# Kernel optimization log

Measured on AMD Instinct MI355X. Metric: run time of the kernel, lower is better.

Reference implementation:

```python
import jax, jax.numpy as jnp
import numpy as np

HEADS = 8  # head_dim = 512 // 8 = 64


def setup_inputs() -> dict:
    key = jax.random.key(0)
    ks = jax.random.split(key, 6)
    B, S, D = 1, 4096, 512
    s = 0.02
    return {
        "hidden_states": jax.random.normal(ks[0], (B, S, D), dtype=jnp.float32),
        "Wq": jax.random.normal(ks[1], (D, D), dtype=jnp.float32) * s,
        "Wk": jax.random.normal(ks[2], (D, D), dtype=jnp.float32) * s,
        "Wv": jax.random.normal(ks[3], (D, D), dtype=jnp.float32) * s,
        "Wo": jax.random.normal(ks[4], (D, D), dtype=jnp.float32) * s,
        "b_out": jnp.zeros((D,), dtype=jnp.float32),
    }


def reference(hidden_states, Wq, Wk, Wv, Wo, b_out):
    B, S, D = hidden_states.shape
    H = HEADS
    hd = D // H
    scale = 1.0 / jnp.sqrt(jnp.asarray(hd, hidden_states.dtype))

    # unfused QKV projections (self-attention, no mask)
    q = hidden_states @ Wq  # [B,S,D]
    k = hidden_states @ Wk
    v = hidden_states @ Wv

    # head_to_batch_dim: [B,S,D] -> [B,H,S,hd]
    def split_heads(t):
        return t.reshape(B, S, H, hd).transpose(0, 2, 1, 3)

    q, k, v = split_heads(q), split_heads(k), split_heads(v)

    # explicit score matrix + softmax (faithful to torch.bmm path)
    scores = jnp.einsum("bhqd,bhkd->bhqk", q, k) * scale  # [B,H,S,S]
    probs = jax.nn.softmax(scores, axis=-1)
    out = jnp.einsum("bhqk,bhkd->bhqd", probs, v)  # [B,H,S,hd]

    # batch_to_head_dim: [B,H,S,hd] -> [B,S,D]
    out = out.transpose(0, 2, 1, 3).reshape(B, S, D)
    # to_out[0] Linear + to_out[1] Dropout (identity at eval)
    return out @ Wo + b_out
```

## Files before the change

kernel.cpp:

```cpp
#include <hip/hip_runtime.h>
#include <hip/hip_bf16.h>

#define S_LEN 4096
#define DMODEL 512
#define NHEADS 8
#define HDIM 64

typedef __hip_bfloat16 bf16;
typedef __attribute__((ext_vector_type(8))) short bf16x8;
typedef __attribute__((ext_vector_type(4))) float f32x4;
typedef __attribute__((ext_vector_type(4))) _Float16 f16x4;
typedef __attribute__((ext_vector_type(8))) _Float16 f16x8;

__device__ __forceinline__ f32x4 mfma16x16x32(bf16x8 a, bf16x8 b, f32x4 c) {
    return __builtin_amdgcn_mfma_f32_16x16x32_bf16(a, b, c, 0, 0, 0);
}
__device__ __forceinline__ f32x4 mfma16x16x16h(f16x4 a, f16x4 b, f32x4 c) {
    return __builtin_amdgcn_mfma_f32_16x16x16f16(a, b, c, 0, 0, 0);
}
__device__ __forceinline__ void gload_lds16(const void* g, void* l) {
    __builtin_amdgcn_global_load_lds(
        (const __attribute__((address_space(1))) unsigned int*)g,
        (__attribute__((address_space(3))) unsigned int*)l, 16, 0, 0);
}

__global__ __launch_bounds__(256) void prep(
    const float* __restrict__ X,
    const float* __restrict__ Wq, const float* __restrict__ Wk,
    const float* __restrict__ Wv, const float* __restrict__ Wo,
    bf16* __restrict__ Xb, bf16* __restrict__ Wt)
{
    __shared__ bf16 tile[32][33];
    const int b = blockIdx.x;
    if (b < 1024) {
        int i = (b * 256 + threadIdx.x) * 8;
        float4 a = *(const float4*)(X + i);
        float4 c = *(const float4*)(X + i + 4);
        bf16 tmp[8];
        tmp[0] = __float2bfloat16(a.x); tmp[1] = __float2bfloat16(a.y);
        tmp[2] = __float2bfloat16(a.z); tmp[3] = __float2bfloat16(a.w);
        tmp[4] = __float2bfloat16(c.x); tmp[5] = __float2bfloat16(c.y);
        tmp[6] = __float2bfloat16(c.z); tmp[7] = __float2bfloat16(c.w);
        *(bf16x8*)(Xb + i) = *(bf16x8*)tmp;
    } else {
        const int bb = b - 1024;
        const int z = bb >> 8;
        const int bx = bb & 15, by = (bb >> 4) & 15;
        const float* src = (z == 0) ? Wq : (z == 1) ? Wk : (z == 2) ? Wv : Wo;
        bf16* dst = Wt + (size_t)z * DMODEL * DMODEL;
        const int tx = threadIdx.x & 31, ty = threadIdx.x >> 5;
        const int x = bx * 32 + tx;
        const int y0 = by * 32;
        #pragma unroll
        for (int i = ty; i < 32; i += 8)
            tile[i][tx] = __float2bfloat16(src[(size_t)(y0 + i) * DMODEL + x]);
        __syncthreads();
        const int xo = y0 + tx;
        #pragma unroll
        for (int i = ty; i < 32; i += 8)
            dst[(size_t)(bx * 32 + i) * DMODEL + xo] = tile[tx][i];
    }
}

__global__ __launch_bounds__(256) void gemm_qkv(
    const bf16* __restrict__ A, const bf16* __restrict__ Bt,
    bf16* __restrict__ Qm, bf16* __restrict__ Km, _Float16* __restrict__ Vt)
{
    __shared__ __align__(16) bf16 As[128 * 64];
    __shared__ __align__(16) bf16 Bs[128 * 64];
    const int m0 = blockIdx.x * 128, n0 = blockIdx.y * 128;
    const int t = threadIdx.x, lane = t & 63, w = t >> 6;
    const int lr = lane & 15, lq = lane >> 4;
    const int wr = w >> 1, wc = w & 1;

    f32x4 acc[4][4];
    #pragma unroll
    for (int i = 0; i < 4; ++i)
        #pragma unroll
        for (int j = 0; j < 4; ++j) acc[i][j] = f32x4{0, 0, 0, 0};

    const int srow = w * 32 + (lane >> 3);
    const int scol = (lane & 7) * 8;
    const bf16* Ab = A + (size_t)(m0 + srow) * DMODEL + scol;
    const bf16* Bb = Bt + (size_t)(n0 + srow) * DMODEL + scol;

    for (int k0 = 0; k0 < DMODEL; k0 += 64) {
        __syncthreads();
        #pragma unroll
        for (int i = 0; i < 4; ++i) {
            gload_lds16(Ab + (size_t)(i * 8) * DMODEL + k0, &As[(w * 32 + i * 8) * 64]);
            gload_lds16(Bb + (size_t)(i * 8) * DMODEL + k0, &Bs[(w * 32 + i * 8) * 64]);
        }
        __syncthreads();
        #pragma unroll
        for (int kc = 0; kc < 2; ++kc) {
            bf16x8 af[4], bfr[4];
            #pragma unroll
            for (int fq = 0; fq < 4; ++fq)
                af[fq] = *(const bf16x8*)&As[(wr * 64 + fq * 16 + lr) * 64 + kc * 32 + lq * 8];
            #pragma unroll
            for (int fr = 0; fr < 4; ++fr)
                bfr[fr] = *(const bf16x8*)&Bs[(wc * 64 + fr * 16 + lr) * 64 + kc * 32 + lq * 8];
            #pragma unroll
            for (int fq = 0; fq < 4; ++fq)
                #pragma unroll
                for (int fr = 0; fr < 4; ++fr)
                    acc[fq][fr] = mfma16x16x32(af[fq], bfr[fr], acc[fq][fr]);
        }
    }

    const int which = n0 >> 9;
    const int nloc = n0 & 511;
    const int row0 = m0 + wr * 64 + lq * 4;
    const int col0 = nloc + wc * 64 + lr;
    if (which == 0) {
        #pragma unroll
        for (int fq = 0; fq < 4; ++fq)
            #pragma unroll
            for (int fr = 0; fr < 4; ++fr)
                #pragma unroll
                for (int r = 0; r < 4; ++r)
                    Qm[(size_t)(row0 + fq * 16 + r) * DMODEL + col0 + fr * 16] =
                        __float2bfloat16(acc[fq][fr][r] * 0.18033688f);
    } else if (which == 1) {
        #pragma unroll
        for (int fq = 0; fq < 4; ++fq)
            #pragma unroll
            for (int fr = 0; fr < 4; ++fr)
                #pragma unroll
                for (int r = 0; r < 4; ++r)
                    Km[(size_t)(row0 + fq * 16 + r) * DMODEL + col0 + fr * 16] =
                        __float2bfloat16(acc[fq][fr][r]);
    } else {
        #pragma unroll
        for (int fq = 0; fq < 4; ++fq)
            #pragma unroll
            for (int fr = 0; fr < 4; ++fr) {
                _Float16 tmp[4];
                #pragma unroll
                for (int r = 0; r < 4; ++r) tmp[r] = (_Float16)acc[fq][fr][r];
                *(f16x4*)(Vt + (size_t)(col0 + fr * 16) * S_LEN + row0 + fq * 16) =
                    *(f16x4*)tmp;
            }
    }
}

__global__ __launch_bounds__(256) void gemm_out(
    const bf16* __restrict__ A, const bf16* __restrict__ Bt,
    float* __restrict__ Out, const float* __restrict__ bias)
{
    __shared__ __align__(16) bf16 As[128 * 64];
    __shared__ __align__(16) bf16 Bs[128 * 64];
    const int m0 = blockIdx.x * 128, n0 = blockIdx.y * 128;
    const int t = threadIdx.x, lane = t & 63, w = t >> 6;
    const int lr = lane & 15, lq = lane >> 4;
    const int wr = w >> 1, wc = w & 1;

    f32x4 acc[4][4];
    #pragma unroll
    for (int i = 0; i < 4; ++i)
        #pragma unroll
        for (int j = 0; j < 4; ++j) acc[i][j] = f32x4{0, 0, 0, 0};

    const int srow = w * 32 + (lane >> 3);
    const int scol = (lane & 7) * 8;
    const bf16* Ab = A + (size_t)(m0 + srow) * DMODEL + scol;
    const bf16* Bb = Bt + (size_t)(n0 + srow) * DMODEL + scol;

    for (int k0 = 0; k0 < DMODEL; k0 += 64) {
        __syncthreads();
        #pragma unroll
        for (int i = 0; i < 4; ++i) {
            gload_lds16(Ab + (size_t)(i * 8) * DMODEL + k0, &As[(w * 32 + i * 8) * 64]);
            gload_lds16(Bb + (size_t)(i * 8) * DMODEL + k0, &Bs[(w * 32 + i * 8) * 64]);
        }
        __syncthreads();
        #pragma unroll
        for (int kc = 0; kc < 2; ++kc) {
            bf16x8 af[4], bfr[4];
            #pragma unroll
            for (int fq = 0; fq < 4; ++fq)
                af[fq] = *(const bf16x8*)&As[(wr * 64 + fq * 16 + lr) * 64 + kc * 32 + lq * 8];
            #pragma unroll
            for (int fr = 0; fr < 4; ++fr)
                bfr[fr] = *(const bf16x8*)&Bs[(wc * 64 + fr * 16 + lr) * 64 + kc * 32 + lq * 8];
            #pragma unroll
            for (int fq = 0; fq < 4; ++fq)
                #pragma unroll
                for (int fr = 0; fr < 4; ++fr)
                    acc[fq][fr] = mfma16x16x32(af[fq], bfr[fr], acc[fq][fr]);
        }
    }

    const int row0 = m0 + wr * 64 + lq * 4;
    const int col0 = n0 + wc * 64 + lr;
    #pragma unroll
    for (int fq = 0; fq < 4; ++fq)
        #pragma unroll
        for (int fr = 0; fr < 4; ++fr)
            #pragma unroll
            for (int r = 0; r < 4; ++r)
                Out[(size_t)(row0 + fq * 16 + r) * DMODEL + col0 + fr * 16] =
                    acc[fq][fr][r] + bias[col0 + fr * 16];
}

__global__ __launch_bounds__(256, 2) void attn_kernel(
    const bf16* __restrict__ Q, const bf16* __restrict__ Kmat,
    const _Float16* __restrict__ Vt, bf16* __restrict__ Oout)
{
    __shared__ __align__(16) char smem[65536];

    const int h = blockIdx.x, qb = blockIdx.y;
    const int t = threadIdx.x, lane = t & 63, w = t >> 6;
    const int lr = lane & 15, lq = lane >> 4;
    const int q0 = qb * 64;

    char* myK = smem + w * 16384;
    char* myV = myK + 8192;

    const int sr = lane >> 3;
    const int scc = (lane & 7) ^ sr;
    const bf16*     gK = Kmat + (size_t)sr * DMODEL + h * HDIM + scc * 8;
    const _Float16* gV = Vt + (size_t)(h * HDIM + sr) * S_LEN + scc * 8;

    bf16x8 qf[4][2];
    #pragma unroll
    for (int qt = 0; qt < 4; ++qt) {
        const bf16* qp = Q + (size_t)(q0 + qt * 16 + lr) * DMODEL + h * HDIM + lq * 8;
        qf[qt][0] = *(const bf16x8*)qp;
        qf[qt][1] = *(const bf16x8*)(qp + 32);
    }

    f32x4 oacc[4][4];
    #pragma unroll
    for (int i = 0; i < 4; ++i)
        #pragma unroll
        for (int j = 0; j < 4; ++j) oacc[i][j] = f32x4{0, 0, 0, 0};
    float lsum[4] = {0, 0, 0, 0};

    #pragma unroll
    for (int i = 0; i < 8; ++i) {
        gload_lds16(gK + (size_t)(w * 64 + i * 8) * DMODEL, myK + i * 1024);
        gload_lds16(gV + (size_t)(i * 8) * S_LEN + w * 64, myV + i * 1024);
    }

    const int swz = (lr & 7) << 4;

    for (int kt = w; kt < S_LEN / 64; kt += 4) {
        asm volatile("s_waitcnt vmcnt(0)" ::: "memory");

        bf16x8 kf[4][2];
        #pragma unroll
        for (int mt = 0; mt < 4; ++mt) {
            const char* kr = myK + (mt * 16 + lr) * 128;
            kf[mt][0] = *(const bf16x8*)(kr + ((lq * 16) ^ swz));
            kf[mt][1] = *(const bf16x8*)(kr + ((64 + lq * 16) ^ swz));
        }
        f16x4 vf[4][4];
        #pragma unroll
        for (int ht = 0; ht < 4; ++ht) {
            const char* vr = myV + (ht * 16 + lr) * 128;
            #pragma unroll
            for (int mt = 0; mt < 4; ++mt)
                vf[mt][ht] = *(const f16x4*)(vr + ((mt * 32 + lq * 8) ^ swz));
        }
        asm volatile("s_waitcnt lgkmcnt(0)" ::: "memory");
        __builtin_amdgcn_sched_barrier(0);

        const int ktn = kt + 4;
        if (ktn < S_LEN / 64) {
            #pragma unroll
            for (int i = 0; i < 8; ++i) {
                gload_lds16(gK + (size_t)(ktn * 64 + i * 8) * DMODEL, myK + i * 1024);
                gload_lds16(gV + (size_t)(i * 8) * S_LEN + ktn * 64, myV + i * 1024);
            }
        }

        __builtin_amdgcn_s_setprio(1);
        f16x4 pf[4][4];
        #pragma unroll
        for (int qt = 0; qt < 4; ++qt) {
            f32x4 st[4];
            #pragma unroll
            for (int mt = 0; mt < 4; ++mt) {
                f32x4 z = {0, 0, 0, 0};
                z = mfma16x16x32(kf[mt][0], qf[qt][0], z);
                z = mfma16x16x32(kf[mt][1], qf[qt][1], z);
                st[mt] = z;
            }
            #pragma unroll
            for (int mt = 0; mt < 4; ++mt)
                #pragma unroll
                for (int r = 0; r < 4; ++r) {
                    float p = __builtin_amdgcn_exp2f(st[mt][r]);
                    lsum[qt] += p;
                    pf[qt][mt][r] = (_Float16)p;
                }
        }
        #pragma unroll
        for (int qt = 0; qt < 4; ++qt)
            #pragma unroll
            for (int ht = 0; ht < 4; ++ht)
                #pragma unroll
                for (int mt = 0; mt < 4; ++mt)
                    oacc[qt][ht] = mfma16x16x16h(pf[qt][mt], vf[mt][ht], oacc[qt][ht]);
        __builtin_amdgcn_s_setprio(0);
    }

    __syncthreads();
    float (*obuf)[3][4][64][4] = (float(*)[3][4][64][4])smem;
    float (*lbuf)[4][16]       = (float(*)[4][16])(smem + 49152);

    #pragma unroll
    for (int qt = 0; qt < 4; ++qt) {
        if (qt != w) {
            int j = qt - (qt > w ? 1 : 0);
            #pragma unroll
            for (int ht = 0; ht < 4; ++ht)
                *(f32x4*)&obuf[w][j][ht][lane][0] = oacc[qt][ht];
        }
    }
    #pragma unroll
    for (int qt = 0; qt < 4; ++qt) {
        float s = lsum[qt];
        s += __shfl_xor(s, 16);
        s += __shfl_xor(s, 32);
        if (lq == 0) lbuf[w][qt][lr] = s;
    }
    __syncthreads();

    f32x4 osum[4];
    #pragma unroll
    for (int qt = 0; qt < 4; ++qt)
        if (qt == w) {
            #pragma unroll
            for (int ht = 0; ht < 4; ++ht) osum[ht] = oacc[qt][ht];
        }
    #pragma unroll
    for (int w2 = 0; w2 < 4; ++w2) {
        if (w2 == w) continue;
        int j = w - (w > w2 ? 1 : 0);
        #pragma unroll
        for (int ht = 0; ht < 4; ++ht)
            osum[ht] += *(const f32x4*)&obuf[w2][j][ht][lane][0];
    }
    float linv[4];
    #pragma unroll
    for (int r = 0; r < 4; ++r) {
        int rr = lq * 4 + r;
        linv[r] = 1.0f / (lbuf[0][w][rr] + lbuf[1][w][rr] + lbuf[2][w][rr] + lbuf[3][w][rr]);
    }
    #pragma unroll
    for (int r = 0; r < 4; ++r) {
        int row = q0 + w * 16 + lq * 4 + r;
        #pragma unroll
        for (int ht = 0; ht < 4; ++ht)
            Oout[(size_t)row * DMODEL + h * HDIM + ht * 16 + lr] =
                __float2bfloat16(osum[ht][r] * linv[r]);
    }
}

extern "C" void kernel_launch(void* const* d_in, const int* in_sizes, int n_in,
                              void* d_out, int out_size, void* d_ws, size_t ws_size,
                              hipStream_t stream) {
    const float* X  = (const float*)d_in[0];
    const float* Wq = (const float*)d_in[1];
    const float* Wk = (const float*)d_in[2];
    const float* Wv = (const float*)d_in[3];
    const float* Wo = (const float*)d_in[4];
    const float* bo = (const float*)d_in[5];
    float* out = (float*)d_out;

    char* ws = (char*)d_ws;
    bf16* Wt = (bf16*)ws;
    bf16* Xb = (bf16*)(ws + (size_t)4 * DMODEL * DMODEL * 2);
    bf16* Qm = Xb + (size_t)S_LEN * DMODEL;
    bf16* Km = Qm + (size_t)S_LEN * DMODEL;
    _Float16* Vt = (_Float16*)(Km + (size_t)S_LEN * DMODEL);
    bf16* AO = (bf16*)(Vt + (size_t)S_LEN * DMODEL);

    bf16* Wot = Wt + (size_t)3 * DMODEL * DMODEL;

    prep<<<2048, 256, 0, stream>>>(X, Wq, Wk, Wv, Wo, Xb, Wt);

    gemm_qkv<<<dim3(S_LEN / 128, 3 * DMODEL / 128), 256, 0, stream>>>(
        Xb, Wt, Qm, Km, Vt);

    attn_kernel<<<dim3(NHEADS, S_LEN / 64), 256, 0, stream>>>(Qm, Km, Vt, AO);

    gemm_out<<<dim3(S_LEN / 128, DMODEL / 128), 256, 0, stream>>>(AO, Wot, out, bo);
}
```

Measured before the change: 139.5 us.

## Shrink GEMM tiles with double buffering, MFMA row sums, vectorized V loads

Both projection GEMMs move from 128x128 to 64x64 tiles with a double-buffered LDS prefetch pipeline, giving more blocks to fill the many CUs at this small problem size. The V-transpose epilogue now goes through LDS so global stores are coalesced. In attention, the softmax row sums are computed with an extra MFMA against a ones vector instead of scalar adds and shuffles, and V fragments are loaded as wider 8-element reads. The smaller tiles lower data reuse per block and the extra MFMAs add matrix work to the attention loop.

```diff
diff --git a/kernel.cpp b/kernel.cpp
--- a/kernel.cpp
+++ b/kernel.cpp
@@ -18,6 +18,8 @@
 __device__ __forceinline__ f32x4 mfma16x16x16h(f16x4 a, f16x4 b, f32x4 c) {
     return __builtin_amdgcn_mfma_f32_16x16x16f16(a, b, c, 0, 0, 0);
 }
+__device__ __forceinline__ f16x4 lo4(f16x8 v) { return __builtin_shufflevector(v, v, 0, 1, 2, 3); }
+__device__ __forceinline__ f16x4 hi4(f16x8 v) { return __builtin_shufflevector(v, v, 4, 5, 6, 7); }
 __device__ __forceinline__ void gload_lds16(const void* g, void* l) {
     __builtin_amdgcn_global_load_lds(
         (const __attribute__((address_space(1))) unsigned int*)g,
@@ -66,82 +68,89 @@
     const bf16* __restrict__ A, const bf16* __restrict__ Bt,
     bf16* __restrict__ Qm, bf16* __restrict__ Km, _Float16* __restrict__ Vt)
 {
-    __shared__ __align__(16) bf16 As[128 * 64];
-    __shared__ __align__(16) bf16 Bs[128 * 64];
-    const int m0 = blockIdx.x * 128, n0 = blockIdx.y * 128;
+    __shared__ __align__(16) bf16 As[2][64 * 64];
+    __shared__ __align__(16) bf16 Bs[2][64 * 64];
+    const int m0 = blockIdx.x * 64, n0 = blockIdx.y * 64;
     const int t = threadIdx.x, lane = t & 63, w = t >> 6;
     const int lr = lane & 15, lq = lane >> 4;
-    const int wr = w >> 1, wc = w & 1;
-
-    f32x4 acc[4][4];
-    #pragma unroll
-    for (int i = 0; i < 4; ++i)
-        #pragma unroll
-        for (int j = 0; j < 4; ++j) acc[i][j] = f32x4{0, 0, 0, 0};
-
-    const int srow = w * 32 + (lane >> 3);
+
+    f32x4 acc[4] = {f32x4{0,0,0,0}, f32x4{0,0,0,0}, f32x4{0,0,0,0}, f32x4{0,0,0,0}};
+
+    const int srow = w * 8 + (lane >> 3);
     const int scol = (lane & 7) * 8;
     const bf16* Ab = A + (size_t)(m0 + srow) * DMODEL + scol;
     const bf16* Bb = Bt + (size_t)(n0 + srow) * DMODEL + scol;
-
-    for (int k0 = 0; k0 < DMODEL; k0 += 64) {
-        __syncthreads();
-        #pragma unroll
-        for (int i = 0; i < 4; ++i) {
-            gload_lds16(Ab + (size_t)(i * 8) * DMODEL + k0, &As[(w * 32 + i * 8) * 64]);
-            gload_lds16(Bb + (size_t)(i * 8) * DMODEL + k0, &Bs[(w * 32 + i * 8) * 64]);
-        }
-        __syncthreads();
+    const int lb = (w * 8) * 64;
+
+#define QKV_STAGE(k0, bsel) do {                                        \
+        gload_lds16(Ab + (k0), &As[bsel][lb]);                          \
+        gload_lds16(Ab + 32 * DMODEL + (k0), &As[bsel][lb + 32 * 64]);  \
+        gload_lds16(Bb + (k0), &Bs[bsel][lb]);                          \
+        gload_lds16(Bb + 32 * DMODEL + (k0), &Bs[bsel][lb + 32 * 64]);  \
+    } while (0)
+
+    QKV_STAGE(0, 0);
+    #pragma unroll
+    for (int ks = 0; ks < 8; ++ks) {
+        const int cur = ks & 1;
+        if (ks < 7) {
+            QKV_STAGE((ks + 1) * 64, cur ^ 1);
+            asm volatile("s_waitcnt vmcnt(4)" ::: "memory");
+        } else {
+            asm volatile("s_waitcnt vmcnt(0)" ::: "memory");
+        }
+        __builtin_amdgcn_s_barrier();
+        __builtin_amdgcn_sched_barrier(0);
         #pragma unroll
         for (int kc = 0; kc < 2; ++kc) {
-            bf16x8 af[4], bfr[4];
-            #pragma unroll
-            for (int fq = 0; fq < 4; ++fq)
-                af[fq] = *(const bf16x8*)&As[(wr * 64 + fq * 16 + lr) * 64 + kc * 32 + lq * 8];
-            #pragma unroll
-            for (int fr = 0; fr < 4; ++fr)
-                bfr[fr] = *(const bf16x8*)&Bs[(wc * 64 + fr * 16 + lr) * 64 + kc * 32 + lq * 8];
-            #pragma unroll
-            for (int fq = 0; fq < 4; ++fq)
-                #pragma unroll
-                for (int fr = 0; fr < 4; ++fr)
-                    acc[fq][fr] = mfma16x16x32(af[fq], bfr[fr], acc[fq][fr]);
-        }
-    }
+            bf16x8 a = *(const bf16x8*)&As[cur][(w * 16 + lr) * 64 + kc * 32 + lq * 8];
+            #pragma unroll
+            for (int nt = 0; nt < 4; ++nt) {
+                bf16x8 b = *(const bf16x8*)&Bs[cur][(nt * 16 + lr) * 64 + kc * 32 + lq * 8];
+                acc[nt] = mfma16x16x32(a, b, acc[nt]);
+            }
+        }
+        asm volatile("s_waitcnt lgkmcnt(0)" ::: "memory");
+        __builtin_amdgcn_sched_barrier(0);
+        __builtin_amdgcn_s_barrier();
+    }
+#undef QKV_STAGE
 
     const int which = n0 >> 9;
     const int nloc = n0 & 511;
-    const int row0 = m0 + wr * 64 + lq * 4;
-    const int col0 = nloc + wc * 64 + lr;
     if (which == 0) {
         #pragma unroll
-        for (int fq = 0; fq < 4; ++fq)
-            #pragma unroll
-            for (int fr = 0; fr < 4; ++fr)
-                #pragma unroll
-                for (int r = 0; r < 4; ++r)
-                    Qm[(size_t)(row0 + fq * 16 + r) * DMODEL + col0 + fr * 16] =
-                        __float2bfloat16(acc[fq][fr][r] * 0.18033688f);
+        for (int nt = 0; nt < 4; ++nt)
+            #pragma unroll
+            for (int r = 0; r < 4; ++r)
+                Qm[(size_t)(m0 + w * 16 + lq * 4 + r) * DMODEL + nloc + nt * 16 + lr] =
+                    __float2bfloat16(acc[nt][r] * 0.18033688f);
     } else if (which == 1) {
         #pragma unroll
-        for (int fq = 0; fq < 4; ++fq)
-            #pragma unroll
-            for (int fr = 0; fr < 4; ++fr)
-                #pragma unroll
-                for (int r = 0; r < 4; ++r)
-                    Km[(size_t)(row0 + fq * 16 + r) * DMODEL + col0 + fr * 16] =
-                        __float2bfloat16(acc[fq][fr][r]);
+        for (int nt = 0; nt < 4; ++nt)
+            #pragma unroll
+            for (int r = 0; r < 4; ++r)
+                Km[(size_t)(m0 + w * 16 + lq * 4 + r) * DMODEL + nloc + nt * 16 + lr] =
+                    __float2bfloat16(acc[nt][r]);
     } else {
-        #pragma unroll
-        for (int fq = 0; fq < 4; ++fq)
-            #pragma unroll
-            for (int fr = 0; fr < 4; ++fr) {
-                _Float16 tmp[4];
-                #pragma unroll
-                for (int r = 0; r < 4; ++r) tmp[r] = (_Float16)acc[fq][fr][r];
-                *(f16x4*)(Vt + (size_t)(col0 + fr * 16) * S_LEN + row0 + fq * 16) =
-                    *(f16x4*)tmp;
-            }
+        _Float16* tb = (_Float16*)As;
+        #pragma unroll
+        for (int nt = 0; nt < 4; ++nt)
+            #pragma unroll
+            for (int r = 0; r < 4; ++r)
+                tb[(w * 16 + lq * 4 + r) * 72 + nt * 16 + lr] = (_Float16)acc[nt][r];
+        __syncthreads();
+        const int c = t >> 2, seg = t & 3;
+        _Float16 tmp[16];
+        #pragma unroll
+        for (int j = 0; j < 16; ++j)
+            tmp[j] = tb[(seg * 16 + j) * 72 + c];
+        _Float16* vp = Vt + (size_t)(nloc + c) * S_LEN + m0;
+        #pragma unroll
+        for (int g = 0; g < 4; ++g) {
+            f16x4 vv = {tmp[g * 4 + 0], tmp[g * 4 + 1], tmp[g * 4 + 2], tmp[g * 4 + 3]};
+            *(f16x4*)(vp + g * 16 + seg * 4) = vv;
+        }
     }
 }
 
@@ -149,59 +158,60 @@
     const bf16* __restrict__ A, const bf16* __restrict__ Bt,
     float* __restrict__ Out, const float* __restrict__ bias)
 {
-    __shared__ __align__(16) bf16 As[128 * 64];
-    __shared__ __align__(16) bf16 Bs[128 * 64];
-    const int m0 = blockIdx.x * 128, n0 = blockIdx.y * 128;
+    __shared__ __align__(16) bf16 As[2][64 * 64];
+    __shared__ __align__(16) bf16 Bs[2][64 * 64];
+    const int m0 = blockIdx.x * 64, n0 = blockIdx.y * 64;
     const int t = threadIdx.x, lane = t & 63, w = t >> 6;
     const int lr = lane & 15, lq = lane >> 4;
-    const int wr = w >> 1, wc = w & 1;
-
-    f32x4 acc[4][4];
-    #pragma unroll
-    for (int i = 0; i < 4; ++i)
-        #pragma unroll
-        for (int j = 0; j < 4; ++j) acc[i][j] = f32x4{0, 0, 0, 0};
-
-    const int srow = w * 32 + (lane >> 3);
+
+    f32x4 acc[4] = {f32x4{0,0,0,0}, f32x4{0,0,0,0}, f32x4{0,0,0,0}, f32x4{0,0,0,0}};
+
+    const int srow = w * 8 + (lane >> 3);
     const int scol = (lane & 7) * 8;
     const bf16* Ab = A + (size_t)(m0 + srow) * DMODEL + scol;
     const bf16* Bb = Bt + (size_t)(n0 + srow) * DMODEL + scol;
-
-    for (int k0 = 0; k0 < DMODEL; k0 += 64) {
-        __syncthreads();
-        #pragma unroll
-        for (int i = 0; i < 4; ++i) {
-            gload_lds16(Ab + (size_t)(i * 8) * DMODEL + k0, &As[(w * 32 + i * 8) * 64]);
-            gload_lds16(Bb + (size_t)(i * 8) * DMODEL + k0, &Bs[(w * 32 + i * 8) * 64]);
-        }
-        __syncthreads();
+    const int lb = (w * 8) * 64;
+
+#define OUT_STAGE(k0, bsel) do {                                        \
+        gload_lds16(Ab + (k0), &As[bsel][lb]);                          \
+        gload_lds16(Ab + 32 * DMODEL + (k0), &As[bsel][lb + 32 * 64]);  \
+        gload_lds16(Bb + (k0), &Bs[bsel][lb]);                          \
+        gload_lds16(Bb + 32 * DMODEL + (k0), &Bs[bsel][lb + 32 * 64]);  \
+    } while (0)
+
+    OUT_STAGE(0, 0);
+    #pragma unroll
+    for (int ks = 0; ks < 8; ++ks) {
+        const int cur = ks & 1;
+        if (ks < 7) {
+            OUT_STAGE((ks + 1) * 64, cur ^ 1);
+            asm volatile("s_waitcnt vmcnt(4)" ::: "memory");
+        } else {
+            asm volatile("s_waitcnt vmcnt(0)" ::: "memory");
+        }
+        __builtin_amdgcn_s_barrier();
+        __builtin_amdgcn_sched_barrier(0);
         #pragma unroll
         for (int kc = 0; kc < 2; ++kc) {
-            bf16x8 af[4], bfr[4];
-            #pragma unroll
-            for (int fq = 0; fq < 4; ++fq)
-                af[fq] = *(const bf16x8*)&As[(wr * 64 + fq * 16 + lr) * 64 + kc * 32 + lq * 8];
-            #pragma unroll
-            for (int fr = 0; fr < 4; ++fr)
-                bfr[fr] = *(const bf16x8*)&Bs[(wc * 64 + fr * 16 + lr) * 64 + kc * 32 + lq * 8];
-            #pragma unroll
-            for (int fq = 0; fq < 4; ++fq)
-                #pragma unroll
-                for (int fr = 0; fr < 4; ++fr)
-                    acc[fq][fr] = mfma16x16x32(af[fq], bfr[fr], acc[fq][fr]);
-        }
-    }
-
-    const int row0 = m0 + wr * 64 + lq * 4;
-    const int col0 = n0 + wc * 64 + lr;
-    #pragma unroll
-    for (int fq = 0; fq < 4; ++fq)
-        #pragma unroll
-        for (int fr = 0; fr < 4; ++fr)
-            #pragma unroll
-            for (int r = 0; r < 4; ++r)
-                Out[(size_t)(row0 + fq * 16 + r) * DMODEL + col0 + fr * 16] =
-                    acc[fq][fr][r] + bias[col0 + fr * 16];
+            bf16x8 a = *(const bf16x8*)&As[cur][(w * 16 + lr) * 64 + kc * 32 + lq * 8];
+            #pragma unroll
+            for (int nt = 0; nt < 4; ++nt) {
+                bf16x8 b = *(const bf16x8*)&Bs[cur][(nt * 16 + lr) * 64 + kc * 32 + lq * 8];
+                acc[nt] = mfma16x16x32(a, b, acc[nt]);
+            }
+        }
+        asm volatile("s_waitcnt lgkmcnt(0)" ::: "memory");
+        __builtin_amdgcn_sched_barrier(0);
+        __builtin_amdgcn_s_barrier();
+    }
+#undef OUT_STAGE
+
+    #pragma unroll
+    for (int nt = 0; nt < 4; ++nt)
+        #pragma unroll
+        for (int r = 0; r < 4; ++r)
+            Out[(size_t)(m0 + w * 16 + lq * 4 + r) * DMODEL + n0 + nt * 16 + lr] =
+                acc[nt][r] + bias[n0 + nt * 16 + lr];
 }
 
 __global__ __launch_bounds__(256, 2) void attn_kernel(
@@ -236,7 +246,10 @@
     for (int i = 0; i < 4; ++i)
         #pragma unroll
         for (int j = 0; j < 4; ++j) oacc[i][j] = f32x4{0, 0, 0, 0};
-    float lsum[4] = {0, 0, 0, 0};
+    f32x4 lacc[4];
+    #pragma unroll
+    for (int i = 0; i < 4; ++i) lacc[i] = f32x4{0, 0, 0, 0};
+    const f16x4 vones = {(_Float16)1.0f, (_Float16)1.0f, (_Float16)1.0f, (_Float16)1.0f};
 
     #pragma unroll
     for (int i = 0; i < 8; ++i) {
@@ -256,13 +269,12 @@
             kf[mt][0] = *(const bf16x8*)(kr + ((lq * 16) ^ swz));
             kf[mt][1] = *(const bf16x8*)(kr + ((64 + lq * 16) ^ swz));
         }
-        f16x4 vf[4][4];
+        f16x8 vA[4], vB[4];
         #pragma unroll
         for (int ht = 0; ht < 4; ++ht) {
             const char* vr = myV + (ht * 16 + lr) * 128;
-            #pragma unroll
-            for (int mt = 0; mt < 4; ++mt)
-                vf[mt][ht] = *(const f16x4*)(vr + ((mt * 32 + lq * 8) ^ swz));
+            vA[ht] = *(const f16x8*)(vr + ((lq * 32) ^ swz));
+            vB[ht] = *(const f16x8*)(vr + ((lq * 32 + 16) ^ swz));
         }
         asm volatile("s_waitcnt lgkmcnt(0)" ::: "memory");
         __builtin_amdgcn_sched_barrier(0);
@@ -291,19 +303,23 @@
             #pragma unroll
             for (int mt = 0; mt < 4; ++mt)
                 #pragma unroll
-                for (int r = 0; r < 4; ++r) {
-                    float p = __builtin_amdgcn_exp2f(st[mt][r]);
-                    lsum[qt] += p;
-                    pf[qt][mt][r] = (_Float16)p;
-                }
+                for (int r = 0; r < 4; ++r)
+                    pf[qt][mt][r] = (_Float16)__builtin_amdgcn_exp2f(st[mt][r]);
         }
         #pragma unroll
         for (int qt = 0; qt < 4; ++qt)
             #pragma unroll
-            for (int ht = 0; ht < 4; ++ht)
-                #pragma unroll
-                for (int mt = 0; mt < 4; ++mt)
-                    oacc[qt][ht] = mfma16x16x16h(pf[qt][mt], vf[mt][ht], oacc[qt][ht]);
+            for (int ht = 0; ht < 4; ++ht) {
+                oacc[qt][ht] = mfma16x16x16h(pf[qt][0], lo4(vA[ht]), oacc[qt][ht]);
+                oacc[qt][ht] = mfma16x16x16h(pf[qt][1], hi4(vA[ht]), oacc[qt][ht]);
+                oacc[qt][ht] = mfma16x16x16h(pf[qt][2], lo4(vB[ht]), oacc[qt][ht]);
+                oacc[qt][ht] = mfma16x16x16h(pf[qt][3], hi4(vB[ht]), oacc[qt][ht]);
+            }
+        #pragma unroll
+        for (int qt = 0; qt < 4; ++qt)
+            #pragma unroll
+            for (int mt = 0; mt < 4; ++mt)
+                lacc[qt] = mfma16x16x16h(pf[qt][mt], vones, lacc[qt]);
         __builtin_amdgcn_s_setprio(0);
     }
 
@@ -320,12 +336,12 @@
                 *(f32x4*)&obuf[w][j][ht][lane][0] = oacc[qt][ht];
         }
     }
-    #pragma unroll
-    for (int qt = 0; qt < 4; ++qt) {
-        float s = lsum[qt];
-        s += __shfl_xor(s, 16);
-        s += __shfl_xor(s, 32);
-        if (lq == 0) lbuf[w][qt][lr] = s;
+    if (lr == 0) {
+        #pragma unroll
+        for (int qt = 0; qt < 4; ++qt)
+            #pragma unroll
+            for (int r = 0; r < 4; ++r)
+                lbuf[w][qt][lq * 4 + r] = lacc[qt][r];
     }
     __syncthreads();
 
@@ -383,10 +399,10 @@
 
     prep<<<2048, 256, 0, stream>>>(X, Wq, Wk, Wv, Wo, Xb, Wt);
 
-    gemm_qkv<<<dim3(S_LEN / 128, 3 * DMODEL / 128), 256, 0, stream>>>(
+    gemm_qkv<<<dim3(S_LEN / 64, 3 * DMODEL / 64), 256, 0, stream>>>(
         Xb, Wt, Qm, Km, Vt);
 
     attn_kernel<<<dim3(NHEADS, S_LEN / 64), 256, 0, stream>>>(Qm, Km, Vt, AO);
 
-    gemm_out<<<dim3(S_LEN / 128, DMODEL / 128), 256, 0, stream>>>(AO, Wot, out, bo);
-}
+    gemm_out<<<dim3(S_LEN / 64, DMODEL / 64), 256, 0, stream>>>(AO, Wot, out, bo);
+}
```

Result: slower. 144.4 us (+3.4%).
